# Performance work log

Hardware: AMD Instinct MI355X
Metric: run time of the kernel (lower is better)

## Reference

```python
import jax, jax.numpy as jnp
import numpy as np

M_PER_GROUP = 16
EPS = 0.001


def setup_inputs() -> dict:
    key = jax.random.key(0)
    x = jax.random.normal(key, (32, 64, 64, 256), dtype=jnp.float32)
    return {"x": x}


def reference(x) -> jnp.ndarray:
    # x: [B, W, H, C] (NHWC). Training-phase path, decomposition='cholesky', renorm=False.
    b, w, h, c = x.shape
    groups = c // M_PER_GROUP
    n = b * w * h  # samples per channel

    # [C, B*W*H]
    x_flat = jnp.transpose(x, (3, 0, 1, 2)).reshape(c, -1)
    mean = jnp.mean(x_flat, axis=1, keepdims=True)          # [C, 1]
    f = x_flat - mean                                        # [C, N]

    # per-group covariance: [G, m, N] -> [G, m, m]
    fg = f.reshape(groups, M_PER_GROUP, -1)
    denom = jnp.float32(n) - 1.0
    cov = jnp.einsum('gmn,gkn->gmk', fg, fg) / denom
    eye = jnp.eye(M_PER_GROUP, dtype=x.dtype)
    cov = (1.0 - EPS) * cov + EPS * eye
    # NOTE: the original TF code divides by (N-1) a second time after shrinkage;
    # reproduced faithfully here.
    cov = cov / denom

    # batched Cholesky + triangular solve: inv_sqrt = L^{-1}
    chol = jnp.linalg.cholesky(cov)                          # [G, m, m], lower
    inv_sqrt = jax.vmap(
        lambda L: jax.scipy.linalg.solve_triangular(L, eye, lower=True)
    )(chol)                                                  # [G, m, m]

    # whiten: [G, m, m] @ [G, m, N] -> [G, m, N]
    f_hat = jnp.einsum('gmk,gkn->gmn', inv_sqrt, fg)
    out = f_hat.reshape(c, b, w, h)
    return jnp.transpose(out, (1, 2, 3, 0))
```

## Files before the change

kernel.cpp:

```cpp
#include <hip/hip_runtime.h>


#define NROWS   131072
#define DENOMF  131071.0f
#define EPSV    0.001f

#define OFF_INV    0
#define OFF_BIAS   4096
#define OFF_RED3   4352
#define OFF_PART3  17664
#define PWN        832

typedef __attribute__((ext_vector_type(8))) short bf16x8;
typedef __attribute__((ext_vector_type(4))) float f32x4;
typedef __attribute__((ext_vector_type(4))) unsigned int u32x4;

__device__ __forceinline__ unsigned int fbits(float v) {
    return __builtin_bit_cast(unsigned int, v);
}
__device__ __forceinline__ float bfloat(unsigned int u) {
    return __builtin_bit_cast(float, u);
}

struct Row8 { float a, b, c, d, e, f, g, h; };

__device__ __forceinline__ Row8 load8(const float* p) {
    Row8 r;
    r.a = p[0];    r.b = p[256];  r.c = p[512];  r.d = p[768];
    r.e = p[1024]; r.f = p[1280]; r.g = p[1536]; r.h = p[1792];
    return r;
}

__device__ __forceinline__ void cvt8(const Row8 r, bf16x8& hv, bf16x8& lv, float& s) {
    s += ((r.a + r.b) + (r.c + r.d)) + ((r.e + r.f) + (r.g + r.h));
    const unsigned int ua = fbits(r.a), ub = fbits(r.b), uc = fbits(r.c), ud = fbits(r.d);
    const unsigned int ue = fbits(r.e), uf = fbits(r.f), ug = fbits(r.g), uh = fbits(r.h);
    u32x4 hp;
    hp.x = (ub & 0xFFFF0000u) | (ua >> 16);
    hp.y = (ud & 0xFFFF0000u) | (uc >> 16);
    hp.z = (uf & 0xFFFF0000u) | (ue >> 16);
    hp.w = (uh & 0xFFFF0000u) | (ug >> 16);
    const float da = r.a - bfloat(ua & 0xFFFF0000u);
    const float db = r.b - bfloat(ub & 0xFFFF0000u);
    const float dc = r.c - bfloat(uc & 0xFFFF0000u);
    const float dd = r.d - bfloat(ud & 0xFFFF0000u);
    const float de = r.e - bfloat(ue & 0xFFFF0000u);
    const float df = r.f - bfloat(uf & 0xFFFF0000u);
    const float dg = r.g - bfloat(ug & 0xFFFF0000u);
    const float dh = r.h - bfloat(uh & 0xFFFF0000u);
    u32x4 lp;
    lp.x = (fbits(db) & 0xFFFF0000u) | (fbits(da) >> 16);
    lp.y = (fbits(dd) & 0xFFFF0000u) | (fbits(dc) >> 16);
    lp.z = (fbits(df) & 0xFFFF0000u) | (fbits(de) >> 16);
    lp.w = (fbits(dh) & 0xFFFF0000u) | (fbits(dg) >> 16);
    hv = __builtin_bit_cast(bf16x8, hp);
    lv = __builtin_bit_cast(bf16x8, lp);
}

__global__ __launch_bounds__(256, 4) void k1_stats(const float* __restrict__ x,
                                                   float* __restrict__ ws, int NW) {
    const int tid = threadIdx.x;
    const int lane = tid & 63, wv = tid >> 6;
    const int W = blockIdx.x * 4 + wv;
    const int UPW = 65536 / NW;
    const int g = W & 15, strip = W >> 4;
    const int ch = g * 16 + (lane & 15);
    const size_t row0 = (size_t)strip * UPW * 32 + (size_t)((lane >> 4) * 8);
    const float* p = x + row0 * 256 + ch;

    f32x4 aHH = {0.f, 0.f, 0.f, 0.f};
    f32x4 aHL = {0.f, 0.f, 0.f, 0.f};
    f32x4 aLL = {0.f, 0.f, 0.f, 0.f};
    float s = 0.f;

    Row8 c0 = load8(p);
    Row8 c1 = load8(p + 8192);
    for (int u = 0; u < UPW; ++u) {
        const int up = (u + 2 < UPW) ? (u + 2) : (UPW - 1);
        Row8 nx = load8(p + (size_t)up * 8192);
        bf16x8 hv, lv;
        cvt8(c0, hv, lv, s);
        aHH = __builtin_amdgcn_mfma_f32_16x16x32_bf16(hv, hv, aHH, 0, 0, 0);
        aHL = __builtin_amdgcn_mfma_f32_16x16x32_bf16(hv, lv, aHL, 0, 0, 0);
        aLL = __builtin_amdgcn_mfma_f32_16x16x32_bf16(lv, lv, aLL, 0, 0, 0);
        c0 = c1; c1 = nx;
    }

    float* pw = ws + OFF_PART3 + (size_t)W * PWN;
    pw[0 * 64 + lane]  = aHH[0]; pw[1 * 64 + lane]  = aHH[1];
    pw[2 * 64 + lane]  = aHH[2]; pw[3 * 64 + lane]  = aHH[3];
    pw[4 * 64 + lane]  = aHL[0]; pw[5 * 64 + lane]  = aHL[1];
    pw[6 * 64 + lane]  = aHL[2]; pw[7 * 64 + lane]  = aHL[3];
    pw[8 * 64 + lane]  = aLL[0]; pw[9 * 64 + lane]  = aLL[1];
    pw[10 * 64 + lane] = aLL[2]; pw[11 * 64 + lane] = aLL[3];
    pw[12 * 64 + lane] = s;
}

__global__ __launch_bounds__(256, 2) void k2_reduce(float* __restrict__ ws, int NW) {
    const int t = blockIdx.x * 256 + threadIdx.x;
    if (t >= 16 * PWN) return;
    const int g = t / PWN, k = t % PWN;
    const int S = NW / 16;
    const float* p = ws + OFF_PART3 + (size_t)g * PWN + k;
    float sum = 0.f;
#pragma unroll 8
    for (int i = 0; i < S; ++i) sum += p[(size_t)i * 16 * PWN];
    ws[OFF_RED3 + t] = sum;
}

__global__ void k2_chol(float* __restrict__ ws, int NW) {
    __shared__ float sg[PWN];
    const int g = blockIdx.x, tid = threadIdx.x;
    for (int e = tid; e < PWN; e += 64) sg[e] = ws[OFF_RED3 + g * PWN + e];
    __syncthreads();

    const int ii = tid & 15;
    const float inv_denom = 1.0f / DENOMF;
    const float cs_ii = sg[768 + ii] + sg[768 + 16 + ii] +
                        sg[768 + 32 + ii] + sg[768 + 48 + ii];
    const float mu_l = cs_ii * (1.0f / (float)NROWS);

#define GIDX(T, I, J) ((T) * 256 + ((I) & 3) * 64 + ((((I) >> 2)) << 4) + (J))
    float arow[16];
#pragma unroll
    for (int kk = 0; kk < 16; ++kk) {
        float G = sg[GIDX(0, ii, kk)] + sg[GIDX(1, ii, kk)] +
                  sg[GIDX(1, kk, ii)] + sg[GIDX(2, ii, kk)];
        float mu_k = __shfl(mu_l, kk, 64);
        float cv = (G - (float)NROWS * mu_l * mu_k) * inv_denom;
        cv = cv * (1.0f - EPSV) + ((kk == ii) ? EPSV : 0.0f);
        arow[kk] = cv * inv_denom;
    }
#undef GIDX

    float lrow[16];
#pragma unroll
    for (int j = 0; j < 16; ++j) {
        float diag = __shfl(arow[j], j, 64);
        float ljj  = sqrtf(diag);
        float lij  = (ii == j) ? ljj : arow[j] / ljj;
        lrow[j] = lij;
#pragma unroll
        for (int k = j + 1; k < 16; ++k) {
            float lkj = __shfl(lij, k, 64);
            arow[k] = fmaf(-lij, lkj, arow[k]);
        }
    }

    float xcol[16];
#pragma unroll
    for (int i2 = 0; i2 < 16; ++i2) {
        float ssum = (ii == i2) ? 1.0f : 0.0f;
#pragma unroll
        for (int k = 0; k < 16; ++k) {
            if (k < i2) {
                float Lik = __shfl(lrow[k], i2, 64);
                ssum = fmaf(-Lik, xcol[k], ssum);
            }
        }
        float Lii = __shfl(lrow[i2], i2, 64);
        xcol[i2] = (i2 >= ii) ? ssum / Lii : 0.0f;
    }

    float* invg = ws + OFF_INV + g * 256;
#pragma unroll
    for (int i2 = 0; i2 < 16; ++i2) {
        if (tid < 16) invg[i2 * 16 + tid] = xcol[i2];
        float bi = xcol[i2] * mu_l;
        bi += __shfl_xor(bi, 1, 64);
        bi += __shfl_xor(bi, 2, 64);
        bi += __shfl_xor(bi, 4, 64);
        bi += __shfl_xor(bi, 8, 64);
        if (tid == 0) ws[OFF_BIAS + g * 16 + i2] = bi;
    }
}

template <int CTRL>
__device__ __forceinline__ float dpp1(float v) {
    int iv = __builtin_bit_cast(int, v);
    int r = __builtin_amdgcn_update_dpp(iv, iv, CTRL, 0xF, 0xF, false);
    return __builtin_bit_cast(float, r);
}
template <int CTRL>
__device__ __forceinline__ float4 dpp4(float4 v) {
    float4 r;
    r.x = dpp1<CTRL>(v.x);
    r.y = dpp1<CTRL>(v.y);
    r.z = dpp1<CTRL>(v.z);
    r.w = dpp1<CTRL>(v.w);
    return r;
}

#define DOT4(O, A, V) \
    O = fmaf(A.x, V.x, O); O = fmaf(A.y, V.y, O); \
    O = fmaf(A.z, V.z, O); O = fmaf(A.w, V.w, O)

__global__ __launch_bounds__(256, 4) void k3_apply(const float* __restrict__ x,
                                                   const float* __restrict__ ws,
                                                   float* __restrict__ out) {
    const int tid = threadIdx.x, lane = tid & 63, wv = tid >> 6;
    const int q = lane & 3, g = lane >> 2;

    const float* invg = ws + OFF_INV + g * 256;
#define LOADIR(R, M) \
    *reinterpret_cast<const float4*>(invg + (4 * q + (R)) * 16 + 4 * (q ^ (M)))
    float4 ir00 = LOADIR(0, 0), ir01 = LOADIR(0, 1), ir02 = LOADIR(0, 2), ir03 = LOADIR(0, 3);
    float4 ir10 = LOADIR(1, 0), ir11 = LOADIR(1, 1), ir12 = LOADIR(1, 2), ir13 = LOADIR(1, 3);
    float4 ir20 = LOADIR(2, 0), ir21 = LOADIR(2, 1), ir22 = LOADIR(2, 2), ir23 = LOADIR(2, 3);
    float4 ir30 = LOADIR(3, 0), ir31 = LOADIR(3, 1), ir32 = LOADIR(3, 2), ir33 = LOADIR(3, 3);
#undef LOADIR
    float4 b4 = *reinterpret_cast<const float4*>(ws + OFF_BIAS + g * 16 + 4 * q);

    const int rpb   = NROWS / gridDim.x;
    const int iters = rpb / 4;
    const size_t rowbase = (size_t)blockIdx.x * rpb;
    const float4* xp = reinterpret_cast<const float4*>(x) + rowbase * 64 + lane;
    float4*       op = reinterpret_cast<float4*>(out)     + rowbase * 64 + lane;

    float4 cur = xp[(size_t)wv * 64];
    for (int i = 0; i < iters; ++i) {
        const int ip = (i + 1 < iters) ? (i + 1) : (iters - 1);
        float4 nxt = xp[(size_t)(ip * 4 + wv) * 64];

        float4 v0 = cur;
        float4 v1 = dpp4<0xB1>(cur);
        float4 v2 = dpp4<0x4E>(cur);
        float4 v3 = dpp4<0x1B>(cur);

        float o0 = -b4.x, o1 = -b4.y, o2 = -b4.z, o3 = -b4.w;
        DOT4(o0, ir00, v0); DOT4(o0, ir01, v1); DOT4(o0, ir02, v2); DOT4(o0, ir03, v3);
        DOT4(o1, ir10, v0); DOT4(o1, ir11, v1); DOT4(o1, ir12, v2); DOT4(o1, ir13, v3);
        DOT4(o2, ir20, v0); DOT4(o2, ir21, v1); DOT4(o2, ir22, v2); DOT4(o2, ir23, v3);
        DOT4(o3, ir30, v0); DOT4(o3, ir31, v1); DOT4(o3, ir32, v2); DOT4(o3, ir33, v3);

        op[(size_t)(i * 4 + wv) * 64] = make_float4(o0, o1, o2, o3);
        cur = nxt;
    }
}

extern "C" void kernel_launch(void* const* d_in, const int* in_sizes, int n_in,
                              void* d_out, int out_size, void* d_ws, size_t ws_size,
                              hipStream_t stream) {
    const float* x = (const float*)d_in[0];
    float* out = (float*)d_out;
    float* ws  = (float*)d_ws;

    int NW = 1024;
    if (ws_size >= (size_t)(OFF_PART3 + 4096 * PWN) * sizeof(float)) NW = 4096;
    else if (ws_size >= (size_t)(OFF_PART3 + 2048 * PWN) * sizeof(float)) NW = 2048;

    k1_stats<<<NW / 4, 256, 0, stream>>>(x, ws, NW);
    k2_reduce<<<(16 * PWN + 255) / 256, 256, 0, stream>>>(ws, NW);
    k2_chol<<<16, 64, 0, stream>>>(ws, NW);
    k3_apply<<<1024, 256, 0, stream>>>(x, ws, out);
}
```

Baseline: 105.4 us.

## Switch stats Gram to 32x32 MFMA over group pairs with two-stage reduction

The statistics kernel now has each wave cover two adjacent 16-channel groups (32 channels) and uses 32x32x16 bf16 MFMA. Each load therefore spans 32 contiguous channels (128 bytes) instead of 16, which should improve memory coalescing, and prefetch depth goes from 2 to 3. The off-diagonal 16x16 blocks are computed but thrown away. Partials grow fourfold (3136 floats per wave), so the reduction is split across 16 y-slices and finished inside the Cholesky kernel. The cost is extra partial-sum traffic and a larger workspace, which can lower the NW chosen for the workspace size.

```diff
diff --git a/kernel.cpp b/kernel.cpp
--- a/kernel.cpp
+++ b/kernel.cpp
@@ -7,13 +7,14 @@
 
 #define OFF_INV    0
 #define OFF_BIAS   4096
-#define OFF_RED3   4352
-#define OFF_PART3  17664
-#define PWN        832
-
-typedef __attribute__((ext_vector_type(8))) short bf16x8;
-typedef __attribute__((ext_vector_type(4))) float f32x4;
-typedef __attribute__((ext_vector_type(4))) unsigned int u32x4;
+#define OFF_RED1   4352
+#define OFF_PART3  405760
+#define PWN        3136
+#define GPN        25088
+
+typedef __attribute__((ext_vector_type(8)))  short bf16x8;
+typedef __attribute__((ext_vector_type(16))) float f32x16;
+typedef __attribute__((ext_vector_type(4)))  unsigned int u32x4;
 
 __device__ __forceinline__ unsigned int fbits(float v) {
     return __builtin_bit_cast(unsigned int, v);
@@ -62,76 +63,89 @@
     const int tid = threadIdx.x;
     const int lane = tid & 63, wv = tid >> 6;
     const int W = blockIdx.x * 4 + wv;
-    const int UPW = 65536 / NW;
-    const int g = W & 15, strip = W >> 4;
-    const int ch = g * 16 + (lane & 15);
-    const size_t row0 = (size_t)strip * UPW * 32 + (size_t)((lane >> 4) * 8);
+    const int gp = W & 7, strip = W >> 3;
+    const int RWV = (NROWS * 8) / NW;
+    const int UPW = RWV / 16;
+    const int ch = gp * 32 + (lane & 31);
+    const size_t row0 = (size_t)strip * RWV + (size_t)((lane >> 5) * 8);
     const float* p = x + row0 * 256 + ch;
 
-    f32x4 aHH = {0.f, 0.f, 0.f, 0.f};
-    f32x4 aHL = {0.f, 0.f, 0.f, 0.f};
-    f32x4 aLL = {0.f, 0.f, 0.f, 0.f};
+    f32x16 aHH = {0.f}; f32x16 aHL = {0.f}; f32x16 aLL = {0.f};
+#pragma unroll
+    for (int r = 0; r < 16; ++r) { aHH[r] = 0.f; aHL[r] = 0.f; aLL[r] = 0.f; }
     float s = 0.f;
 
     Row8 c0 = load8(p);
-    Row8 c1 = load8(p + 8192);
+    Row8 c1 = load8(p + 4096);
+    Row8 c2 = load8(p + 8192);
     for (int u = 0; u < UPW; ++u) {
-        const int up = (u + 2 < UPW) ? (u + 2) : (UPW - 1);
-        Row8 nx = load8(p + (size_t)up * 8192);
+        const int up = (u + 3 < UPW) ? (u + 3) : (UPW - 1);
+        Row8 nx = load8(p + (size_t)up * 4096);
         bf16x8 hv, lv;
         cvt8(c0, hv, lv, s);
-        aHH = __builtin_amdgcn_mfma_f32_16x16x32_bf16(hv, hv, aHH, 0, 0, 0);
-        aHL = __builtin_amdgcn_mfma_f32_16x16x32_bf16(hv, lv, aHL, 0, 0, 0);
-        aLL = __builtin_amdgcn_mfma_f32_16x16x32_bf16(lv, lv, aLL, 0, 0, 0);
-        c0 = c1; c1 = nx;
+        aHH = __builtin_amdgcn_mfma_f32_32x32x16_bf16(hv, hv, aHH, 0, 0, 0);
+        aHL = __builtin_amdgcn_mfma_f32_32x32x16_bf16(hv, lv, aHL, 0, 0, 0);
+        aLL = __builtin_amdgcn_mfma_f32_32x32x16_bf16(lv, lv, aLL, 0, 0, 0);
+        c0 = c1; c1 = c2; c2 = nx;
     }
 
     float* pw = ws + OFF_PART3 + (size_t)W * PWN;
-    pw[0 * 64 + lane]  = aHH[0]; pw[1 * 64 + lane]  = aHH[1];
-    pw[2 * 64 + lane]  = aHH[2]; pw[3 * 64 + lane]  = aHH[3];
-    pw[4 * 64 + lane]  = aHL[0]; pw[5 * 64 + lane]  = aHL[1];
-    pw[6 * 64 + lane]  = aHL[2]; pw[7 * 64 + lane]  = aHL[3];
-    pw[8 * 64 + lane]  = aLL[0]; pw[9 * 64 + lane]  = aLL[1];
-    pw[10 * 64 + lane] = aLL[2]; pw[11 * 64 + lane] = aLL[3];
-    pw[12 * 64 + lane] = s;
-}
-
-__global__ __launch_bounds__(256, 2) void k2_reduce(float* __restrict__ ws, int NW) {
+#pragma unroll
+    for (int r = 0; r < 16; ++r) {
+        pw[(r)      * 64 + lane] = aHH[r];
+        pw[(16 + r) * 64 + lane] = aHL[r];
+        pw[(32 + r) * 64 + lane] = aLL[r];
+    }
+    pw[48 * 64 + lane] = s;
+}
+
+__global__ __launch_bounds__(256, 4) void k2_reduce(float* __restrict__ ws, int NW) {
     const int t = blockIdx.x * 256 + threadIdx.x;
-    if (t >= 16 * PWN) return;
-    const int g = t / PWN, k = t % PWN;
-    const int S = NW / 16;
-    const float* p = ws + OFF_PART3 + (size_t)g * PWN + k;
+    if (t >= GPN) return;
+    const int gp = t / PWN, e = t % PWN;
+    const int S16 = (NW / 8) / 16;
+    const int s0 = blockIdx.y * S16;
+    const float* p = ws + OFF_PART3 + ((size_t)(s0 * 8 + gp)) * PWN + e;
     float sum = 0.f;
 #pragma unroll 8
-    for (int i = 0; i < S; ++i) sum += p[(size_t)i * 16 * PWN];
-    ws[OFF_RED3 + t] = sum;
+    for (int i = 0; i < S16; ++i) sum += p[(size_t)i * 8 * PWN];
+    ws[OFF_RED1 + (size_t)blockIdx.y * GPN + t] = sum;
 }
 
 __global__ void k2_chol(float* __restrict__ ws, int NW) {
     __shared__ float sg[PWN];
     const int g = blockIdx.x, tid = threadIdx.x;
-    for (int e = tid; e < PWN; e += 64) sg[e] = ws[OFF_RED3 + g * PWN + e];
+    const int gp = g >> 1, h = g & 1;
+
+    for (int e = tid; e < PWN; e += 64) {
+        float v = 0.f;
+#pragma unroll
+        for (int y = 0; y < 16; ++y)
+            v += ws[OFF_RED1 + (size_t)y * GPN + gp * PWN + e];
+        sg[e] = v;
+    }
     __syncthreads();
 
     const int ii = tid & 15;
     const float inv_denom = 1.0f / DENOMF;
-    const float cs_ii = sg[768 + ii] + sg[768 + 16 + ii] +
-                        sg[768 + 32 + ii] + sg[768 + 48 + ii];
+    const int c32 = 16 * h + ii;
+    const float cs_ii = sg[48 * 64 + c32] + sg[48 * 64 + 32 + c32];
     const float mu_l = cs_ii * (1.0f / (float)NROWS);
 
-#define GIDX(T, I, J) ((T) * 256 + ((I) & 3) * 64 + ((((I) >> 2)) << 4) + (J))
+#define GIDX32(T, I, J) \
+    ((T) * 1024 + (((I) & 3) + 4 * ((I) >> 3)) * 64 + 32 * (((I) >> 2) & 1) + (J))
     float arow[16];
 #pragma unroll
     for (int kk = 0; kk < 16; ++kk) {
-        float G = sg[GIDX(0, ii, kk)] + sg[GIDX(1, ii, kk)] +
-                  sg[GIDX(1, kk, ii)] + sg[GIDX(2, ii, kk)];
+        const int I = 16 * h + ii, J = 16 * h + kk;
+        float G = sg[GIDX32(0, I, J)] + sg[GIDX32(1, I, J)] +
+                  sg[GIDX32(1, J, I)] + sg[GIDX32(2, I, J)];
         float mu_k = __shfl(mu_l, kk, 64);
         float cv = (G - (float)NROWS * mu_l * mu_k) * inv_denom;
         cv = cv * (1.0f - EPSV) + ((kk == ii) ? EPSV : 0.0f);
         arow[kk] = cv * inv_denom;
     }
-#undef GIDX
+#undef GIDX32
 
     float lrow[16];
 #pragma unroll
@@ -250,7 +264,8 @@
     else if (ws_size >= (size_t)(OFF_PART3 + 2048 * PWN) * sizeof(float)) NW = 2048;
 
     k1_stats<<<NW / 4, 256, 0, stream>>>(x, ws, NW);
-    k2_reduce<<<(16 * PWN + 255) / 256, 256, 0, stream>>>(ws, NW);
+    dim3 rg((GPN + 255) / 256, 16);
+    k2_reduce<<<rg, 256, 0, stream>>>(ws, NW);
     k2_chol<<<16, 64, 0, stream>>>(ws, NW);
     k3_apply<<<1024, 256, 0, stream>>>(x, ws, out);
 }
```

After: 115.5 us, median of 2. 1.1x slower.

## Stage coalesced row tiles through LDS in stats kernel, two-level partial reduction

Applied to the files above, without the earlier changes.

The stats kernel now loads whole 32-row tiles of all 256 channels with coalesced float4 loads into padded shared memory. Each wave then reads strided channel columns from LDS to feed the split-bf16 MFMA covariance accumulation, covering all 16 groups per block instead of one group per wave. This replaces strided scalar global loads that touched only 16 channels per wave. The partial reduction becomes a 2D grid producing 16 intermediate sums that the Cholesky kernel adds itself. The cost is extra LDS traffic, two barriers per tile, and lower occupancy (launch bounds 2).

```diff
diff --git a/kernel.cpp b/kernel.cpp
--- a/kernel.cpp
+++ b/kernel.cpp
@@ -7,9 +7,9 @@
 
 #define OFF_INV    0
 #define OFF_BIAS   4096
-#define OFF_RED3   4352
-#define OFF_PART3  17664
-#define PWN        832
+#define OFF_RED1   4352
+#define OFF_PART4  217344
+#define GSTATS     13312
 
 typedef __attribute__((ext_vector_type(8))) short bf16x8;
 typedef __attribute__((ext_vector_type(4))) float f32x4;
@@ -23,13 +23,6 @@
 }
 
 struct Row8 { float a, b, c, d, e, f, g, h; };
-
-__device__ __forceinline__ Row8 load8(const float* p) {
-    Row8 r;
-    r.a = p[0];    r.b = p[256];  r.c = p[512];  r.d = p[768];
-    r.e = p[1024]; r.f = p[1280]; r.g = p[1536]; r.h = p[1792];
-    return r;
-}
 
 __device__ __forceinline__ void cvt8(const Row8 r, bf16x8& hv, bf16x8& lv, float& s) {
     s += ((r.a + r.b) + (r.c + r.d)) + ((r.e + r.f) + (r.g + r.h));
@@ -57,61 +50,116 @@
     lv = __builtin_bit_cast(bf16x8, lp);
 }
 
-__global__ __launch_bounds__(256, 4) void k1_stats(const float* __restrict__ x,
-                                                   float* __restrict__ ws, int NW) {
+__global__ __launch_bounds__(256, 2) void k1_stats(const float* __restrict__ x,
+                                                   float* __restrict__ ws, int NB) {
+    __shared__ float xt[32 * 260];
     const int tid = threadIdx.x;
     const int lane = tid & 63, wv = tid >> 6;
-    const int W = blockIdx.x * 4 + wv;
-    const int UPW = 65536 / NW;
-    const int g = W & 15, strip = W >> 4;
-    const int ch = g * 16 + (lane & 15);
-    const size_t row0 = (size_t)strip * UPW * 32 + (size_t)((lane >> 4) * 8);
-    const float* p = x + row0 * 256 + ch;
-
-    f32x4 aHH = {0.f, 0.f, 0.f, 0.f};
-    f32x4 aHL = {0.f, 0.f, 0.f, 0.f};
-    f32x4 aLL = {0.f, 0.f, 0.f, 0.f};
-    float s = 0.f;
-
-    Row8 c0 = load8(p);
-    Row8 c1 = load8(p + 8192);
-    for (int u = 0; u < UPW; ++u) {
-        const int up = (u + 2 < UPW) ? (u + 2) : (UPW - 1);
-        Row8 nx = load8(p + (size_t)up * 8192);
-        bf16x8 hv, lv;
-        cvt8(c0, hv, lv, s);
-        aHH = __builtin_amdgcn_mfma_f32_16x16x32_bf16(hv, hv, aHH, 0, 0, 0);
-        aHL = __builtin_amdgcn_mfma_f32_16x16x32_bf16(hv, lv, aHL, 0, 0, 0);
-        aLL = __builtin_amdgcn_mfma_f32_16x16x32_bf16(lv, lv, aLL, 0, 0, 0);
-        c0 = c1; c1 = nx;
-    }
-
-    float* pw = ws + OFF_PART3 + (size_t)W * PWN;
-    pw[0 * 64 + lane]  = aHH[0]; pw[1 * 64 + lane]  = aHH[1];
-    pw[2 * 64 + lane]  = aHH[2]; pw[3 * 64 + lane]  = aHH[3];
-    pw[4 * 64 + lane]  = aHL[0]; pw[5 * 64 + lane]  = aHL[1];
-    pw[6 * 64 + lane]  = aHL[2]; pw[7 * 64 + lane]  = aHL[3];
-    pw[8 * 64 + lane]  = aLL[0]; pw[9 * 64 + lane]  = aLL[1];
-    pw[10 * 64 + lane] = aLL[2]; pw[11 * 64 + lane] = aLL[3];
-    pw[12 * 64 + lane] = s;
-}
-
-__global__ __launch_bounds__(256, 2) void k2_reduce(float* __restrict__ ws, int NW) {
+    const int slot = lane >> 4;
+    const int TPB = (NROWS / 32) / NB;
+    const float4* gf4 = reinterpret_cast<const float4*>(x);
+    const size_t tile0 = (size_t)blockIdx.x * TPB;
+
+    const int rb = wv * 64 + (lane & 15);
+    const int ro0 = (slot * 8 + ((0 + 2 * slot) & 7)) * 260 + rb;
+    const int ro1 = (slot * 8 + ((1 + 2 * slot) & 7)) * 260 + rb;
+    const int ro2 = (slot * 8 + ((2 + 2 * slot) & 7)) * 260 + rb;
+    const int ro3 = (slot * 8 + ((3 + 2 * slot) & 7)) * 260 + rb;
+    const int ro4 = (slot * 8 + ((4 + 2 * slot) & 7)) * 260 + rb;
+    const int ro5 = (slot * 8 + ((5 + 2 * slot) & 7)) * 260 + rb;
+    const int ro6 = (slot * 8 + ((6 + 2 * slot) & 7)) * 260 + rb;
+    const int ro7 = (slot * 8 + ((7 + 2 * slot) & 7)) * 260 + rb;
+
+    f32x4 hh0 = {0,0,0,0}, hl0 = {0,0,0,0}, ll0 = {0,0,0,0};
+    f32x4 hh1 = {0,0,0,0}, hl1 = {0,0,0,0}, ll1 = {0,0,0,0};
+    f32x4 hh2 = {0,0,0,0}, hl2 = {0,0,0,0}, ll2 = {0,0,0,0};
+    f32x4 hh3 = {0,0,0,0}, hl3 = {0,0,0,0}, ll3 = {0,0,0,0};
+    float s0 = 0.f, s1 = 0.f, s2 = 0.f, s3 = 0.f;
+
+    float4 st0, st1, st2, st3, st4, st5, st6, st7;
+#define LOADT(T)                                                              \
+    {                                                                         \
+        const float4* tp = gf4 + (tile0 + (T)) * 2048 + tid;                  \
+        st0 = tp[0];    st1 = tp[256];  st2 = tp[512];  st3 = tp[768];        \
+        st4 = tp[1024]; st5 = tp[1280]; st6 = tp[1536]; st7 = tp[1792];       \
+    }
+#define WRK(K, ST)                                                            \
+    {                                                                         \
+        const int idx = tid + (K) * 256;                                      \
+        *reinterpret_cast<float4*>(&xt[(idx >> 6) * 260 + (idx & 63) * 4]) = ST; \
+    }
+#define PROCG(G, AHH, AHL, ALL, S)                                            \
+    {                                                                         \
+        Row8 r;                                                               \
+        r.a = xt[ro0 + (G) * 16]; r.b = xt[ro1 + (G) * 16];                   \
+        r.c = xt[ro2 + (G) * 16]; r.d = xt[ro3 + (G) * 16];                   \
+        r.e = xt[ro4 + (G) * 16]; r.f = xt[ro5 + (G) * 16];                   \
+        r.g = xt[ro6 + (G) * 16]; r.h = xt[ro7 + (G) * 16];                   \
+        bf16x8 hv, lv;                                                        \
+        cvt8(r, hv, lv, S);                                                   \
+        AHH = __builtin_amdgcn_mfma_f32_16x16x32_bf16(hv, hv, AHH, 0, 0, 0);  \
+        AHL = __builtin_amdgcn_mfma_f32_16x16x32_bf16(hv, lv, AHL, 0, 0, 0);  \
+        ALL = __builtin_amdgcn_mfma_f32_16x16x32_bf16(lv, lv, ALL, 0, 0, 0);  \
+    }
+
+    LOADT(0);
+    for (int t = 0; t < TPB; ++t) {
+        __syncthreads();
+        WRK(0, st0); WRK(1, st1); WRK(2, st2); WRK(3, st3);
+        WRK(4, st4); WRK(5, st5); WRK(6, st6); WRK(7, st7);
+        __syncthreads();
+        const int tn = (t + 1 < TPB) ? (t + 1) : t;
+        LOADT(tn);
+        PROCG(0, hh0, hl0, ll0, s0);
+        PROCG(1, hh1, hl1, ll1, s1);
+        PROCG(2, hh2, hl2, ll2, s2);
+        PROCG(3, hh3, hl3, ll3, s3);
+    }
+#undef PROCG
+#undef WRK
+#undef LOADT
+
+    float* pb = ws + OFF_PART4 + (size_t)blockIdx.x * GSTATS + (size_t)(wv * 4) * 832;
+#define STG(G, AHH, AHL, ALL, S)                                              \
+    {                                                                         \
+        float* pw = pb + (G) * 832;                                           \
+        pw[0 * 64 + lane]  = AHH[0]; pw[1 * 64 + lane]  = AHH[1];             \
+        pw[2 * 64 + lane]  = AHH[2]; pw[3 * 64 + lane]  = AHH[3];             \
+        pw[4 * 64 + lane]  = AHL[0]; pw[5 * 64 + lane]  = AHL[1];             \
+        pw[6 * 64 + lane]  = AHL[2]; pw[7 * 64 + lane]  = AHL[3];             \
+        pw[8 * 64 + lane]  = ALL[0]; pw[9 * 64 + lane]  = ALL[1];             \
+        pw[10 * 64 + lane] = ALL[2]; pw[11 * 64 + lane] = ALL[3];             \
+        pw[12 * 64 + lane] = S;                                               \
+    }
+    STG(0, hh0, hl0, ll0, s0);
+    STG(1, hh1, hl1, ll1, s1);
+    STG(2, hh2, hl2, ll2, s2);
+    STG(3, hh3, hl3, ll3, s3);
+#undef STG
+}
+
+__global__ __launch_bounds__(256, 4) void k2_reduce(float* __restrict__ ws, int NB) {
     const int t = blockIdx.x * 256 + threadIdx.x;
-    if (t >= 16 * PWN) return;
-    const int g = t / PWN, k = t % PWN;
-    const int S = NW / 16;
-    const float* p = ws + OFF_PART3 + (size_t)g * PWN + k;
+    if (t >= GSTATS) return;
+    const int per = NB / 16;
+    const float* p = ws + OFF_PART4 + (size_t)(blockIdx.y * per) * GSTATS + t;
     float sum = 0.f;
 #pragma unroll 8
-    for (int i = 0; i < S; ++i) sum += p[(size_t)i * 16 * PWN];
-    ws[OFF_RED3 + t] = sum;
-}
-
-__global__ void k2_chol(float* __restrict__ ws, int NW) {
-    __shared__ float sg[PWN];
+    for (int b = 0; b < per; ++b) sum += p[(size_t)b * GSTATS];
+    ws[OFF_RED1 + (size_t)blockIdx.y * GSTATS + t] = sum;
+}
+
+__global__ void k2_chol(float* __restrict__ ws, int NB) {
+    __shared__ float sg[832];
     const int g = blockIdx.x, tid = threadIdx.x;
-    for (int e = tid; e < PWN; e += 64) sg[e] = ws[OFF_RED3 + g * PWN + e];
+
+    for (int e = tid; e < 832; e += 64) {
+        float v = 0.f;
+#pragma unroll
+        for (int y = 0; y < 16; ++y)
+            v += ws[OFF_RED1 + (size_t)y * GSTATS + g * 832 + e];
+        sg[e] = v;
+    }
     __syncthreads();
 
     const int ii = tid & 15;
@@ -245,12 +293,13 @@
     float* out = (float*)d_out;
     float* ws  = (float*)d_ws;
 
-    int NW = 1024;
-    if (ws_size >= (size_t)(OFF_PART3 + 4096 * PWN) * sizeof(float)) NW = 4096;
-    else if (ws_size >= (size_t)(OFF_PART3 + 2048 * PWN) * sizeof(float)) NW = 2048;
-
-    k1_stats<<<NW / 4, 256, 0, stream>>>(x, ws, NW);
-    k2_reduce<<<(16 * PWN + 255) / 256, 256, 0, stream>>>(ws, NW);
-    k2_chol<<<16, 64, 0, stream>>>(ws, NW);
+    int NB = 128;
+    if (ws_size >= (size_t)(OFF_PART4 + 512 * GSTATS) * sizeof(float)) NB = 512;
+    else if (ws_size >= (size_t)(OFF_PART4 + 256 * GSTATS) * sizeof(float)) NB = 256;
+
+    k1_stats<<<NB, 256, 0, stream>>>(x, ws, NB);
+    dim3 rg((GSTATS + 255) / 256, 16);
+    k2_reduce<<<rg, 256, 0, stream>>>(ws, NB);
+    k2_chol<<<16, 64, 0, stream>>>(ws, NB);
     k3_apply<<<1024, 256, 0, stream>>>(x, ws, out);
 }
```

After: 98.80 us. 6.3% less time.
